# Kernel tuning notes

Hardware: AMD Instinct MI355X
Metric: run time of the kernel (lower is better)

The kernel has to match this reference:

```python
import jax, jax.numpy as jnp
import numpy as np

B, T, I, H, G = 4096, 1024, 1, 16, 48  # G = 3*H gates

def _gru_layer(inp, w_ih, w_hh, b_ih, b_hh):
    # inp: [B, T, Din] -> out: [B, T, H]. PyTorch GRU gate math.
    # Precompute all input-side gate projections once (batched GEMM).
    xg = jnp.einsum('btd,gd->tbg', inp, w_ih) + b_ih  # [T, B, 3H]

    def step(h, xg_t):
        hg = h @ w_hh.T + b_hh                         # [B, 3H]
        xr, xz, xn = jnp.split(xg_t, 3, axis=-1)
        hr, hz, hn = jnp.split(hg, 3, axis=-1)
        r = jax.nn.sigmoid(xr + hr)
        z = jax.nn.sigmoid(xz + hz)
        n = jnp.tanh(xn + r * hn)
        h_new = (1.0 - z) * n + z * h
        return h_new, h_new

    h0 = jnp.zeros((inp.shape[0], H), dtype=inp.dtype)
    _, ys = jax.lax.scan(step, h0, xg)                 # ys: [T, B, H]
    return jnp.transpose(ys, (1, 0, 2))                # [B, T, H]

def setup_inputs() -> dict:
    key = jax.random.key(0)
    ks = jax.random.split(key, 8)
    s = 1.0 / np.sqrt(H)  # PyTorch default uniform(-1/sqrt(H), 1/sqrt(H))
    u = lambda k, shape: jax.random.uniform(k, shape, jnp.float32, -s, s)
    return {
        'x':      jax.random.normal(ks[0], (B, T, I), jnp.float32),
        'w_ih0':  u(ks[1], (G, I)),
        'w_ih12': u(ks[2], (2, G, H)),
        'w_hh':   u(ks[3], (3, G, H)),
        'b_ih':   u(ks[4], (3, G)),
        'b_hh':   u(ks[5], (3, G)),
        'fc_w':   u(ks[6], (5, H)),
        'fc_b':   u(ks[7], (5,)),
    }

def reference(x, w_ih0, w_ih12, w_hh, b_ih, b_hh, fc_w, fc_b):
    # 3-layer GRU (dropout=0.3 between layers is identity in eval mode)
    h = _gru_layer(x, w_ih0,     w_hh[0], b_ih[0], b_hh[0])
    h = _gru_layer(h, w_ih12[0], w_hh[1], b_ih[1], b_hh[1])
    h = _gru_layer(h, w_ih12[1], w_hh[2], b_ih[2], b_hh[2])
    # Linear head on the last timestep
    return h[:, -1, :] @ fc_w.T + fc_b                 # [B, 5]
```

## Files before the change

### kernel.cpp

```cpp
#include <hip/hip_runtime.h>
#include <stdint.h>

#define TSTEPS 1024
#define S 4
#define NK 258
#define L2E 1.4426950408889634f

typedef float v2f __attribute__((ext_vector_type(2)));
typedef float v4f __attribute__((ext_vector_type(4)));

__device__ __forceinline__ float rcpf_(float v) { return __builtin_amdgcn_rcpf(v); }
__device__ __forceinline__ float ex2(float v) { return __builtin_amdgcn_exp2f(v); }
#define PKFMA(a, b, c) __builtin_elementwise_fma((a), (b), (c))

__device__ __forceinline__ v2f ldg2(const float* p) {
    v2f r; uint64_t a = (uint64_t)p;
    asm volatile("global_load_dwordx2 %0, %1, off\n\ts_waitcnt vmcnt(0)"
                 : "=v"(r) : "v"(a));
    return r;
}
__device__ __forceinline__ float ldg1(const float* p) {
    float r; uint64_t a = (uint64_t)p;
    asm volatile("global_load_dword %0, %1, off\n\ts_waitcnt vmcnt(0)"
                 : "=v"(r) : "v"(a));
    return r;
}

#define RDH(dst, p)                                                        \
    do {                                                                   \
        v4f a0 = *(const v4f*)(p);                                         \
        v4f a1 = *(const v4f*)((p) + 4);                                   \
        v4f a2 = *(const v4f*)((p) + 8);                                   \
        v4f a3 = *(const v4f*)((p) + 12);                                  \
        dst[0] = __builtin_shufflevector(a0, a0, 0, 1);                    \
        dst[1] = __builtin_shufflevector(a0, a0, 2, 3);                    \
        dst[2] = __builtin_shufflevector(a1, a1, 0, 1);                    \
        dst[3] = __builtin_shufflevector(a1, a1, 2, 3);                    \
        dst[4] = __builtin_shufflevector(a2, a2, 0, 1);                    \
        dst[5] = __builtin_shufflevector(a2, a2, 2, 3);                    \
        dst[6] = __builtin_shufflevector(a3, a3, 0, 1);                    \
        dst[7] = __builtin_shufflevector(a3, a3, 2, 3);                    \
    } while (0)

#define DOT8(w, h, seed)                                                   \
    ({                                                                     \
        v2f _a = PKFMA(w[0], h[0], (seed));                                \
        _a = PKFMA(w[1], h[1], _a); _a = PKFMA(w[2], h[2], _a);            \
        _a = PKFMA(w[3], h[3], _a); _a = PKFMA(w[4], h[4], _a);            \
        _a = PKFMA(w[5], h[5], _a); _a = PKFMA(w[6], h[6], _a);            \
        _a = PKFMA(w[7], h[7], _a);                                        \
        _a.x + _a.y;                                                       \
    })

__global__ __launch_bounds__(192, 3)
__attribute__((amdgpu_waves_per_eu(3, 3)))
void gru3_po(
    const float* __restrict__ x,
    const float* __restrict__ w_ih0,
    const float* __restrict__ w_ih12,
    const float* __restrict__ w_hh,
    const float* __restrict__ b_ih,
    const float* __restrict__ b_hh,
    const float* __restrict__ fc_w,
    const float* __restrict__ fc_b,
    float* __restrict__ out)
{
    __shared__ float pring[2][2][S][4][48];
    __shared__ float hscr[3][4][16];

    const int tid = threadIdx.x;
    const int role = tid >> 6;
    const int lane = tid & 63;
    const int s = lane >> 4;
    const int u = lane & 15;
    const int seq = blockIdx.x * 4 + s;

    ((float*)hscr)[tid] = 0.f;
    __syncthreads();

    if (role == 0) {
        v2f wr[8], wz[8], wn[8], v1r[8], v1z[8], v1n[8];
#pragma unroll
        for (int m = 0; m < 8; ++m) {
            wr[m] = ldg2(w_hh + (u) * 16 + 2 * m) * -L2E;
            wz[m] = ldg2(w_hh + (16 + u) * 16 + 2 * m) * -L2E;
            wn[m] = ldg2(w_hh + (32 + u) * 16 + 2 * m) * (2.f * L2E);
            v1r[m] = ldg2(w_ih12 + (u) * 16 + 2 * m) * -L2E;
            v1z[m] = ldg2(w_ih12 + (16 + u) * 16 + 2 * m) * -L2E;
            v1n[m] = ldg2(w_ih12 + (32 + u) * 16 + 2 * m) * (2.f * L2E);
        }
        const float wxr = ldg1(w_ih0 + u) * -L2E;
        const float wxz = ldg1(w_ih0 + 16 + u) * -L2E;
        const float wxn = ldg1(w_ih0 + 32 + u) * (2.f * L2E);
        const v2f sbr = {-(ldg1(b_ih + u) + ldg1(b_hh + u)) * L2E, 0.f};
        const v2f sbz = {-(ldg1(b_ih + 16 + u) + ldg1(b_hh + 16 + u)) * L2E, 0.f};
        const v2f sbn = {ldg1(b_hh + 32 + u) * (2.f * L2E), 0.f};
        const float bnx = ldg1(b_ih + 32 + u) * (2.f * L2E);
        const v2f s1r = {-(ldg1(b_ih + 48 + u) + ldg1(b_hh + 48 + u)) * L2E, 0.f};
        const v2f s1z = {-(ldg1(b_ih + 64 + u) + ldg1(b_hh + 64 + u)) * L2E, 0.f};
        const v2f s1x = {ldg1(b_ih + 80 + u) * (2.f * L2E), 0.f};

        const float* xp = x + (size_t)seq * TSTEPS;
        const float* hr = &hscr[0][s][0];
        float* pc = &pring[0][0][0][s][0];
        float* pp = &pring[0][1][0][s][0];
        float hown = 0.f;
        v4f xq = *(const v4f*)xp;
        for (int K = 0; K < NK; ++K) {
            if (K < 256) {
                v4f xqn = *(const v4f*)(xp + 4 * ((K < 255) ? K + 1 : 255));
#pragma unroll
                for (int j = 0; j < S; ++j) {
                    v2f hp[8];
                    RDH(hp, hr);
                    float xt = xq[j];
                    float sr = fmaf(wxr, xt, DOT8(wr, hp, sbr));
                    float sz = fmaf(wxz, xt, DOT8(wz, hp, sbz));
                    float snh = DOT8(wn, hp, sbn);
                    float r = rcpf_(1.f + ex2(sr));
                    float z = rcpf_(1.f + ex2(sz));
                    float ut = fmaf(r, snh, fmaf(wxn, xt, bnx));
                    float n = fmaf(-2.f, rcpf_(ex2(ut) + 1.f), 1.f);
                    hown = fmaf(z, hown - n, n);
                    hscr[0][s][u] = hown;
                    v2f hq[8];
                    RDH(hq, hr);
                    float pr = DOT8(v1r, hq, s1r);
                    float pz = DOT8(v1z, hq, s1z);
                    float px = DOT8(v1n, hq, s1x);
                    float* pb = pc + j * (4 * 48);
                    pb[u] = pr; pb[16 + u] = pz; pb[32 + u] = px;
                }
                xq = xqn;
            }
            __syncthreads();
            float* t_ = pc; pc = pp; pp = t_;
        }
    } else if (role == 1) {
        v2f wr[8], wz[8], wn[8], v2r[8], v2z[8], v2n[8];
#pragma unroll
        for (int m = 0; m < 8; ++m) {
            wr[m] = ldg2(w_hh + (48 + u) * 16 + 2 * m) * -L2E;
            wz[m] = ldg2(w_hh + (48 + 16 + u) * 16 + 2 * m) * -L2E;
            wn[m] = ldg2(w_hh + (48 + 32 + u) * 16 + 2 * m) * (2.f * L2E);
            v2r[m] = ldg2(w_ih12 + (48 + u) * 16 + 2 * m) * -L2E;
            v2z[m] = ldg2(w_ih12 + (48 + 16 + u) * 16 + 2 * m) * -L2E;
            v2n[m] = ldg2(w_ih12 + (48 + 32 + u) * 16 + 2 * m) * (2.f * L2E);
        }
        const v2f sbn = {ldg1(b_hh + 80 + u) * (2.f * L2E), 0.f};
        const v2f s2r = {-(ldg1(b_ih + 96 + u) + ldg1(b_hh + 96 + u)) * L2E, 0.f};
        const v2f s2z = {-(ldg1(b_ih + 112 + u) + ldg1(b_hh + 112 + u)) * L2E, 0.f};
        const v2f s2x = {ldg1(b_ih + 128 + u) * (2.f * L2E), 0.f};

        const float* hr = &hscr[1][s][0];
        const float* in0 = &pring[0][0][0][s][0];
        const float* in1 = &pring[0][1][0][s][0];
        float* my0 = &pring[1][0][0][s][0];
        float* my1 = &pring[1][1][0][s][0];
        const float* inp = in1;
        float* mycur = my0; float* myprv = my1;
        float hown = 0.f;
        for (int K = 0; K < NK; ++K) {
            if (K >= 1 && K < 257) {
#pragma unroll
                for (int j = 0; j < S; ++j) {
                    const float* qb = inp + j * (4 * 48);
                    float pr = qb[u], pz = qb[16 + u], px = qb[32 + u];
                    v2f hp[8];
                    RDH(hp, hr);
                    float sr = DOT8(wr, hp, ((v2f){pr, 0.f}));
                    float sz = DOT8(wz, hp, ((v2f){pz, 0.f}));
                    float snh = DOT8(wn, hp, sbn);
                    float r = rcpf_(1.f + ex2(sr));
                    float z = rcpf_(1.f + ex2(sz));
                    float ut = fmaf(r, snh, px);
                    float n = fmaf(-2.f, rcpf_(ex2(ut) + 1.f), 1.f);
                    hown = fmaf(z, hown - n, n);
                    hscr[1][s][u] = hown;
                    v2f hq[8];
                    RDH(hq, hr);
                    float qr = DOT8(v2r, hq, s2r);
                    float qz = DOT8(v2z, hq, s2z);
                    float qx = DOT8(v2n, hq, s2x);
                    float* pb = mycur + j * (4 * 48);
                    pb[u] = qr; pb[16 + u] = qz; pb[32 + u] = qx;
                }
            }
            __syncthreads();
            const float* t0 = (inp == in0) ? in1 : in0; inp = t0;
            float* t1 = mycur; mycur = myprv; myprv = t1;
        }
    } else {
        v2f wr[8], wz[8], wn[8];
#pragma unroll
        for (int m = 0; m < 8; ++m) {
            wr[m] = ldg2(w_hh + (96 + u) * 16 + 2 * m) * -L2E;
            wz[m] = ldg2(w_hh + (96 + 16 + u) * 16 + 2 * m) * -L2E;
            wn[m] = ldg2(w_hh + (96 + 32 + u) * 16 + 2 * m) * (2.f * L2E);
        }
        const v2f sbn = {ldg1(b_hh + 128 + u) * (2.f * L2E), 0.f};

        const float* hr = &hscr[2][s][0];
        const float* in0 = &pring[1][0][0][s][0];
        const float* in1 = &pring[1][1][0][s][0];
        const float* inp = in1;
        float hown = 0.f;
        for (int K = 0; K < NK; ++K) {
            if (K >= 2) {
#pragma unroll
                for (int j = 0; j < S; ++j) {
                    const float* qb = inp + j * (4 * 48);
                    float pr = qb[u], pz = qb[16 + u], px = qb[32 + u];
                    v2f hp[8];
                    RDH(hp, hr);
                    float sr = DOT8(wr, hp, ((v2f){pr, 0.f}));
                    float sz = DOT8(wz, hp, ((v2f){pz, 0.f}));
                    float snh = DOT8(wn, hp, sbn);
                    float r = rcpf_(1.f + ex2(sr));
                    float z = rcpf_(1.f + ex2(sz));
                    float ut = fmaf(r, snh, px);
                    float n = fmaf(-2.f, rcpf_(ex2(ut) + 1.f), 1.f);
                    hown = fmaf(z, hown - n, n);
                    hscr[2][s][u] = hown;
                }
            }
            __syncthreads();
            const float* t0 = (inp == in0) ? in1 : in0; inp = t0;
        }
        v2f hf[8];
        RDH(hf, hr);
        const int ur = (u < 5) ? u : 0;
        v2f fw[8];
#pragma unroll
        for (int m = 0; m < 8; ++m) fw[m] = ldg2(fc_w + ur * 16 + 2 * m);
        float acc = ldg1(fc_b + ur) + DOT8(fw, hf, ((v2f){0.f, 0.f}));
        if (u < 5) out[seq * 5 + u] = acc;
    }
}

extern "C" void kernel_launch(void* const* d_in, const int* in_sizes, int n_in,
                              void* d_out, int out_size, void* d_ws, size_t ws_size,
                              hipStream_t stream) {
    const float* x      = (const float*)d_in[0];
    const float* w_ih0  = (const float*)d_in[1];
    const float* w_ih12 = (const float*)d_in[2];
    const float* w_hh   = (const float*)d_in[3];
    const float* b_ih   = (const float*)d_in[4];
    const float* b_hh   = (const float*)d_in[5];
    const float* fc_w   = (const float*)d_in[6];
    const float* fc_b   = (const float*)d_in[7];
    float* out = (float*)d_out;

    gru3_po<<<1024, 192, 0, stream>>>(
        x, w_ih0, w_ih12, w_hh, b_ih, b_hh, fc_w, fc_b, out);
}
```

Baseline: 511.8 us.

## Replace block barriers with LDS flag handshakes and a 4-deep ring between layer waves

Each GRU layer runs on its own wavefront. The per-chunk __syncthreads that lock-stepped all three waves is replaced by producer/consumer counters in shared memory, which are spin-polled with s_sleep. The projection ring buffers grow from 2 to 4 slots, so a producer can run up to four chunks ahead of its consumer, which should absorb load imbalance between layers. The cost is polling overhead. Correctness now depends on LDS write visibility through lgkmcnt waits, with no explicit memory fences.

```diff
diff --git a/kernel.cpp b/kernel.cpp
--- a/kernel.cpp
+++ b/kernel.cpp
@@ -3,7 +3,8 @@
 
 #define TSTEPS 1024
 #define S 4
-#define NK 258
+#define NKA 256
+#define RD 4
 #define L2E 1.4426950408889634f
 
 typedef float v2f __attribute__((ext_vector_type(2)));
@@ -12,6 +13,7 @@
 __device__ __forceinline__ float rcpf_(float v) { return __builtin_amdgcn_rcpf(v); }
 __device__ __forceinline__ float ex2(float v) { return __builtin_amdgcn_exp2f(v); }
 #define PKFMA(a, b, c) __builtin_elementwise_fma((a), (b), (c))
+#define LGKM0() asm volatile("s_waitcnt lgkmcnt(0)" ::: "memory")
 
 __device__ __forceinline__ v2f ldg2(const float* p) {
     v2f r; uint64_t a = (uint64_t)p;
@@ -54,7 +56,7 @@
 
 __global__ __launch_bounds__(192, 3)
 __attribute__((amdgpu_waves_per_eu(3, 3)))
-void gru3_po(
+void gru3_async(
     const float* __restrict__ x,
     const float* __restrict__ w_ih0,
     const float* __restrict__ w_ih12,
@@ -65,9 +67,11 @@
     const float* __restrict__ fc_b,
     float* __restrict__ out)
 {
-    __shared__ float pring[2][2][S][4][48];
+    __shared__ float pring[2][RD][S][4][48];
     __shared__ float hscr[3][4][16];
-
+    __shared__ int flg[4];
+
+    volatile int* vf = flg;
     const int tid = threadIdx.x;
     const int role = tid >> 6;
     const int lane = tid & 63;
@@ -76,6 +80,7 @@
     const int seq = blockIdx.x * 4 + s;
 
     ((float*)hscr)[tid] = 0.f;
+    if (tid < 4) flg[tid] = 0;
     __syncthreads();
 
     if (role == 0) {
@@ -102,39 +107,39 @@
 
         const float* xp = x + (size_t)seq * TSTEPS;
         const float* hr = &hscr[0][s][0];
-        float* pc = &pring[0][0][0][s][0];
-        float* pp = &pring[0][1][0][s][0];
+        float* ring0 = &pring[0][0][0][0][0];
         float hown = 0.f;
         v4f xq = *(const v4f*)xp;
-        for (int K = 0; K < NK; ++K) {
-            if (K < 256) {
-                v4f xqn = *(const v4f*)(xp + 4 * ((K < 255) ? K + 1 : 255));
-#pragma unroll
-                for (int j = 0; j < S; ++j) {
-                    v2f hp[8];
-                    RDH(hp, hr);
-                    float xt = xq[j];
-                    float sr = fmaf(wxr, xt, DOT8(wr, hp, sbr));
-                    float sz = fmaf(wxz, xt, DOT8(wz, hp, sbz));
-                    float snh = DOT8(wn, hp, sbn);
-                    float r = rcpf_(1.f + ex2(sr));
-                    float z = rcpf_(1.f + ex2(sz));
-                    float ut = fmaf(r, snh, fmaf(wxn, xt, bnx));
-                    float n = fmaf(-2.f, rcpf_(ex2(ut) + 1.f), 1.f);
-                    hown = fmaf(z, hown - n, n);
-                    hscr[0][s][u] = hown;
-                    v2f hq[8];
-                    RDH(hq, hr);
-                    float pr = DOT8(v1r, hq, s1r);
-                    float pz = DOT8(v1z, hq, s1z);
-                    float px = DOT8(v1n, hq, s1x);
-                    float* pb = pc + j * (4 * 48);
-                    pb[u] = pr; pb[16 + u] = pz; pb[32 + u] = px;
-                }
-                xq = xqn;
+        for (int K = 0; K < NKA; ++K) {
+            while (vf[2] + RD <= K) __builtin_amdgcn_s_sleep(1);
+            v4f xqn = *(const v4f*)(xp + 4 * ((K < 255) ? K + 1 : 255));
+            float* pb = ring0 + (K & (RD - 1)) * 768 + s * 48;
+#pragma unroll
+            for (int j = 0; j < S; ++j) {
+                v2f hp[8];
+                RDH(hp, hr);
+                float xt = xq[j];
+                float sr = fmaf(wxr, xt, DOT8(wr, hp, sbr));
+                float sz = fmaf(wxz, xt, DOT8(wz, hp, sbz));
+                float snh = DOT8(wn, hp, sbn);
+                float r = rcpf_(1.f + ex2(sr));
+                float z = rcpf_(1.f + ex2(sz));
+                float ut = fmaf(r, snh, fmaf(wxn, xt, bnx));
+                float n = fmaf(-2.f, rcpf_(ex2(ut) + 1.f), 1.f);
+                hown = fmaf(z, hown - n, n);
+                hscr[0][s][u] = hown;
+                v2f hq[8];
+                RDH(hq, hr);
+                float pr = DOT8(v1r, hq, s1r);
+                float pz = DOT8(v1z, hq, s1z);
+                float px = DOT8(v1n, hq, s1x);
+                pb[j * 192 + u] = pr;
+                pb[j * 192 + 16 + u] = pz;
+                pb[j * 192 + 32 + u] = px;
             }
-            __syncthreads();
-            float* t_ = pc; pc = pp; pp = t_;
+            xq = xqn;
+            LGKM0();
+            if (tid == 0) vf[0] = K + 1;
         }
     } else if (role == 1) {
         v2f wr[8], wz[8], wn[8], v2r[8], v2z[8], v2n[8];
@@ -153,42 +158,41 @@
         const v2f s2x = {ldg1(b_ih + 128 + u) * (2.f * L2E), 0.f};
 
         const float* hr = &hscr[1][s][0];
-        const float* in0 = &pring[0][0][0][s][0];
-        const float* in1 = &pring[0][1][0][s][0];
-        float* my0 = &pring[1][0][0][s][0];
-        float* my1 = &pring[1][1][0][s][0];
-        const float* inp = in1;
-        float* mycur = my0; float* myprv = my1;
+        const float* ring0 = &pring[0][0][0][0][0];
+        float* ring1 = &pring[1][0][0][0][0];
         float hown = 0.f;
-        for (int K = 0; K < NK; ++K) {
-            if (K >= 1 && K < 257) {
-#pragma unroll
-                for (int j = 0; j < S; ++j) {
-                    const float* qb = inp + j * (4 * 48);
-                    float pr = qb[u], pz = qb[16 + u], px = qb[32 + u];
-                    v2f hp[8];
-                    RDH(hp, hr);
-                    float sr = DOT8(wr, hp, ((v2f){pr, 0.f}));
-                    float sz = DOT8(wz, hp, ((v2f){pz, 0.f}));
-                    float snh = DOT8(wn, hp, sbn);
-                    float r = rcpf_(1.f + ex2(sr));
-                    float z = rcpf_(1.f + ex2(sz));
-                    float ut = fmaf(r, snh, px);
-                    float n = fmaf(-2.f, rcpf_(ex2(ut) + 1.f), 1.f);
-                    hown = fmaf(z, hown - n, n);
-                    hscr[1][s][u] = hown;
-                    v2f hq[8];
-                    RDH(hq, hr);
-                    float qr = DOT8(v2r, hq, s2r);
-                    float qz = DOT8(v2z, hq, s2z);
-                    float qx = DOT8(v2n, hq, s2x);
-                    float* pb = mycur + j * (4 * 48);
-                    pb[u] = qr; pb[16 + u] = qz; pb[32 + u] = qx;
-                }
+        for (int K = 0; K < NKA; ++K) {
+            while (vf[0] < K + 1) __builtin_amdgcn_s_sleep(1);
+            while (vf[3] + RD <= K) __builtin_amdgcn_s_sleep(1);
+            const float* qb = ring0 + (K & (RD - 1)) * 768 + s * 48;
+            float* pb = ring1 + (K & (RD - 1)) * 768 + s * 48;
+#pragma unroll
+            for (int j = 0; j < S; ++j) {
+                float pr = qb[j * 192 + u];
+                float pz = qb[j * 192 + 16 + u];
+                float px = qb[j * 192 + 32 + u];
+                v2f hp[8];
+                RDH(hp, hr);
+                float sr = DOT8(wr, hp, ((v2f){pr, 0.f}));
+                float sz = DOT8(wz, hp, ((v2f){pz, 0.f}));
+                float snh = DOT8(wn, hp, sbn);
+                float r = rcpf_(1.f + ex2(sr));
+                float z = rcpf_(1.f + ex2(sz));
+                float ut = fmaf(r, snh, px);
+                float n = fmaf(-2.f, rcpf_(ex2(ut) + 1.f), 1.f);
+                hown = fmaf(z, hown - n, n);
+                hscr[1][s][u] = hown;
+                v2f hq[8];
+                RDH(hq, hr);
+                float qr = DOT8(v2r, hq, s2r);
+                float qz = DOT8(v2z, hq, s2z);
+                float qx = DOT8(v2n, hq, s2x);
+                pb[j * 192 + u] = qr;
+                pb[j * 192 + 16 + u] = qz;
+                pb[j * 192 + 32 + u] = qx;
             }
-            __syncthreads();
-            const float* t0 = (inp == in0) ? in1 : in0; inp = t0;
-            float* t1 = mycur; mycur = myprv; myprv = t1;
+            LGKM0();
+            if (tid == 64) { vf[2] = K + 1; vf[1] = K + 1; }
         }
     } else {
         v2f wr[8], wz[8], wn[8];
@@ -201,31 +205,30 @@
         const v2f sbn = {ldg1(b_hh + 128 + u) * (2.f * L2E), 0.f};
 
         const float* hr = &hscr[2][s][0];
-        const float* in0 = &pring[1][0][0][s][0];
-        const float* in1 = &pring[1][1][0][s][0];
-        const float* inp = in1;
+        const float* ring1 = &pring[1][0][0][0][0];
         float hown = 0.f;
-        for (int K = 0; K < NK; ++K) {
-            if (K >= 2) {
-#pragma unroll
-                for (int j = 0; j < S; ++j) {
-                    const float* qb = inp + j * (4 * 48);
-                    float pr = qb[u], pz = qb[16 + u], px = qb[32 + u];
-                    v2f hp[8];
-                    RDH(hp, hr);
-                    float sr = DOT8(wr, hp, ((v2f){pr, 0.f}));
-                    float sz = DOT8(wz, hp, ((v2f){pz, 0.f}));
-                    float snh = DOT8(wn, hp, sbn);
-                    float r = rcpf_(1.f + ex2(sr));
-                    float z = rcpf_(1.f + ex2(sz));
-                    float ut = fmaf(r, snh, px);
-                    float n = fmaf(-2.f, rcpf_(ex2(ut) + 1.f), 1.f);
-                    hown = fmaf(z, hown - n, n);
-                    hscr[2][s][u] = hown;
-                }
+        for (int K = 0; K < NKA; ++K) {
+            while (vf[1] < K + 1) __builtin_amdgcn_s_sleep(1);
+            const float* qb = ring1 + (K & (RD - 1)) * 768 + s * 48;
+#pragma unroll
+            for (int j = 0; j < S; ++j) {
+                float pr = qb[j * 192 + u];
+                float pz = qb[j * 192 + 16 + u];
+                float px = qb[j * 192 + 32 + u];
+                v2f hp[8];
+                RDH(hp, hr);
+                float sr = DOT8(wr, hp, ((v2f){pr, 0.f}));
+                float sz = DOT8(wz, hp, ((v2f){pz, 0.f}));
+                float snh = DOT8(wn, hp, sbn);
+                float r = rcpf_(1.f + ex2(sr));
+                float z = rcpf_(1.f + ex2(sz));
+                float ut = fmaf(r, snh, px);
+                float n = fmaf(-2.f, rcpf_(ex2(ut) + 1.f), 1.f);
+                hown = fmaf(z, hown - n, n);
+                hscr[2][s][u] = hown;
             }
-            __syncthreads();
-            const float* t0 = (inp == in0) ? in1 : in0; inp = t0;
+            LGKM0();
+            if (tid == 128) vf[3] = K + 1;
         }
         v2f hf[8];
         RDH(hf, hr);
@@ -251,6 +254,6 @@
     const float* fc_b   = (const float*)d_in[7];
     float* out = (float*)d_out;
 
-    gru3_po<<<1024, 192, 0, stream>>>(
+    gru3_async<<<1024, 192, 0, stream>>>(
         x, w_ih0, w_ih12, w_hh, b_ih, b_hh, fc_w, fc_b, out);
 }
```

Result: slower. 525.6 us (+2.7%).

## Split each hidden unit's dot products across lane pairs with DPP reduction

Applied to the files above, without the earlier changes.

Each hidden unit is now handled by two lanes, each doing half of the 16-wide dot products, with the partial sums combined through a DPP lane swap. The sigmoid work for r and z is split between the pair and exchanged the same way. Each block now covers 2 sequences instead of 4, the grid doubles, and launch bounds allow 6 blocks per SM. The aim is a shorter serial dependency chain per timestep and more waves to hide latency, at the cost of extra DPP and select instructions and the same number of barriers per sequence.

```diff
diff --git a/kernel.cpp b/kernel.cpp
--- a/kernel.cpp
+++ b/kernel.cpp
@@ -12,6 +12,15 @@
 __device__ __forceinline__ float rcpf_(float v) { return __builtin_amdgcn_rcpf(v); }
 __device__ __forceinline__ float ex2(float v) { return __builtin_amdgcn_exp2f(v); }
 #define PKFMA(a, b, c) __builtin_elementwise_fma((a), (b), (c))
+
+__device__ __forceinline__ float dpp_x1(float v) {
+    return __int_as_float(__builtin_amdgcn_update_dpp(
+        0, __float_as_int(v), 0xB1, 0xF, 0xF, true));
+}
+__device__ __forceinline__ float pairsum(v2f a) {
+    float s = a.x + a.y;
+    return s + dpp_x1(s);
+}
 
 __device__ __forceinline__ v2f ldg2(const float* p) {
     v2f r; uint64_t a = (uint64_t)p;
@@ -26,35 +35,20 @@
     return r;
 }
 
-#define RDH(dst, p)                                                        \
+#define CH4(W, H, SEED) \
+    PKFMA(W[3], H[3], PKFMA(W[2], H[2], PKFMA(W[1], H[1], PKFMA(W[0], H[0], (SEED)))))
+
+#define RD2(dst, p)                                                        \
     do {                                                                   \
         v4f a0 = *(const v4f*)(p);                                         \
         v4f a1 = *(const v4f*)((p) + 4);                                   \
-        v4f a2 = *(const v4f*)((p) + 8);                                   \
-        v4f a3 = *(const v4f*)((p) + 12);                                  \
         dst[0] = __builtin_shufflevector(a0, a0, 0, 1);                    \
         dst[1] = __builtin_shufflevector(a0, a0, 2, 3);                    \
         dst[2] = __builtin_shufflevector(a1, a1, 0, 1);                    \
         dst[3] = __builtin_shufflevector(a1, a1, 2, 3);                    \
-        dst[4] = __builtin_shufflevector(a2, a2, 0, 1);                    \
-        dst[5] = __builtin_shufflevector(a2, a2, 2, 3);                    \
-        dst[6] = __builtin_shufflevector(a3, a3, 0, 1);                    \
-        dst[7] = __builtin_shufflevector(a3, a3, 2, 3);                    \
     } while (0)
 
-#define DOT8(w, h, seed)                                                   \
-    ({                                                                     \
-        v2f _a = PKFMA(w[0], h[0], (seed));                                \
-        _a = PKFMA(w[1], h[1], _a); _a = PKFMA(w[2], h[2], _a);            \
-        _a = PKFMA(w[3], h[3], _a); _a = PKFMA(w[4], h[4], _a);            \
-        _a = PKFMA(w[5], h[5], _a); _a = PKFMA(w[6], h[6], _a);            \
-        _a = PKFMA(w[7], h[7], _a);                                        \
-        _a.x + _a.y;                                                       \
-    })
-
-__global__ __launch_bounds__(192, 3)
-__attribute__((amdgpu_waves_per_eu(3, 3)))
-void gru3_po(
+__global__ __launch_bounds__(192, 6) void gru3_rs32(
     const float* __restrict__ x,
     const float* __restrict__ w_ih0,
     const float* __restrict__ w_ih12,
@@ -65,176 +59,203 @@
     const float* __restrict__ fc_b,
     float* __restrict__ out)
 {
-    __shared__ float pring[2][2][S][4][48];
-    __shared__ float hscr[3][4][16];
+    __shared__ float pring[2][2][S][2][48];
+    __shared__ float hrec[3][2][16];
 
     const int tid = threadIdx.x;
     const int role = tid >> 6;
-    const int lane = tid & 63;
-    const int s = lane >> 4;
-    const int u = lane & 15;
-    const int seq = blockIdx.x * 4 + s;
-
-    ((float*)hscr)[tid] = 0.f;
+    const int l63 = tid & 63;
+    const int s = l63 >> 5;
+    const int l31 = l63 & 31;
+    const int u = l31 >> 1;
+    const int c = l31 & 1;
+    const int c8 = c * 8;
+    const int seq = blockIdx.x * 2 + s;
+    const v2f zz = {0.f, 0.f};
+
+    if (tid < 96) ((float*)hrec)[tid] = 0.f;
     __syncthreads();
 
     if (role == 0) {
-        v2f wr[8], wz[8], wn[8], v1r[8], v1z[8], v1n[8];
-#pragma unroll
-        for (int m = 0; m < 8; ++m) {
-            wr[m] = ldg2(w_hh + (u) * 16 + 2 * m) * -L2E;
-            wz[m] = ldg2(w_hh + (16 + u) * 16 + 2 * m) * -L2E;
-            wn[m] = ldg2(w_hh + (32 + u) * 16 + 2 * m) * (2.f * L2E);
-            v1r[m] = ldg2(w_ih12 + (u) * 16 + 2 * m) * -L2E;
-            v1z[m] = ldg2(w_ih12 + (16 + u) * 16 + 2 * m) * -L2E;
-            v1n[m] = ldg2(w_ih12 + (32 + u) * 16 + 2 * m) * (2.f * L2E);
+        v2f wr[4], wz[4], wn[4], vr[4], vz[4], vn[4];
+#pragma unroll
+        for (int m = 0; m < 4; ++m) {
+            wr[m] = ldg2(w_hh + (u) * 16 + c8 + 2 * m) * -L2E;
+            wz[m] = ldg2(w_hh + (16 + u) * 16 + c8 + 2 * m) * -L2E;
+            wn[m] = ldg2(w_hh + (32 + u) * 16 + c8 + 2 * m) * (2.f * L2E);
+            vr[m] = ldg2(w_ih12 + (u) * 16 + c8 + 2 * m) * -L2E;
+            vz[m] = ldg2(w_ih12 + (16 + u) * 16 + c8 + 2 * m) * -L2E;
+            vn[m] = ldg2(w_ih12 + (32 + u) * 16 + c8 + 2 * m) * (2.f * L2E);
         }
         const float wxr = ldg1(w_ih0 + u) * -L2E;
         const float wxz = ldg1(w_ih0 + 16 + u) * -L2E;
         const float wxn = ldg1(w_ih0 + 32 + u) * (2.f * L2E);
-        const v2f sbr = {-(ldg1(b_ih + u) + ldg1(b_hh + u)) * L2E, 0.f};
-        const v2f sbz = {-(ldg1(b_ih + 16 + u) + ldg1(b_hh + 16 + u)) * L2E, 0.f};
-        const v2f sbn = {ldg1(b_hh + 32 + u) * (2.f * L2E), 0.f};
+        const v2f sbr = {c ? 0.f : -(ldg1(b_ih + u) + ldg1(b_hh + u)) * L2E, 0.f};
+        const v2f sbz = {c ? 0.f : -(ldg1(b_ih + 16 + u) + ldg1(b_hh + 16 + u)) * L2E, 0.f};
+        const v2f sbn = {c ? 0.f : ldg1(b_hh + 32 + u) * (2.f * L2E), 0.f};
         const float bnx = ldg1(b_ih + 32 + u) * (2.f * L2E);
-        const v2f s1r = {-(ldg1(b_ih + 48 + u) + ldg1(b_hh + 48 + u)) * L2E, 0.f};
-        const v2f s1z = {-(ldg1(b_ih + 64 + u) + ldg1(b_hh + 64 + u)) * L2E, 0.f};
-        const v2f s1x = {ldg1(b_ih + 80 + u) * (2.f * L2E), 0.f};
+        const v2f s1r = {c ? 0.f : -(ldg1(b_ih + 48 + u) + ldg1(b_hh + 48 + u)) * L2E, 0.f};
+        const v2f s1z = {c ? 0.f : -(ldg1(b_ih + 64 + u) + ldg1(b_hh + 64 + u)) * L2E, 0.f};
+        const v2f s1x = {c ? 0.f : ldg1(b_ih + 80 + u) * (2.f * L2E), 0.f};
 
         const float* xp = x + (size_t)seq * TSTEPS;
-        const float* hr = &hscr[0][s][0];
-        float* pc = &pring[0][0][0][s][0];
-        float* pp = &pring[0][1][0][s][0];
+        float* hw = &hrec[0][s][u];
+        const float* hr = &hrec[0][s][c8];
+        float* rw0 = &pring[0][0][0][s][0];
+        float* rw1 = &pring[0][1][0][s][0];
+        v2f hrep[4] = {zz, zz, zz, zz};
         float hown = 0.f;
-        v4f xq = *(const v4f*)xp;
         for (int K = 0; K < NK; ++K) {
             if (K < 256) {
-                v4f xqn = *(const v4f*)(xp + 4 * ((K < 255) ? K + 1 : 255));
+                v4f xq = *(const v4f*)(xp + 4 * K);
+                float* pb = rw0;
 #pragma unroll
                 for (int j = 0; j < S; ++j) {
-                    v2f hp[8];
-                    RDH(hp, hr);
                     float xt = xq[j];
-                    float sr = fmaf(wxr, xt, DOT8(wr, hp, sbr));
-                    float sz = fmaf(wxz, xt, DOT8(wz, hp, sbz));
-                    float snh = DOT8(wn, hp, sbn);
-                    float r = rcpf_(1.f + ex2(sr));
-                    float z = rcpf_(1.f + ex2(sz));
+                    v2f a;
+                    a = CH4(wr, hrep, sbr);
+                    float sr = fmaf(wxr, xt, pairsum(a));
+                    a = CH4(wz, hrep, sbz);
+                    float sz = fmaf(wxz, xt, pairsum(a));
+                    a = CH4(wn, hrep, sbn);
+                    float snh = pairsum(a);
+                    float p = c ? sz : sr;
+                    float sg = rcpf_(1.f + ex2(p));
+                    float og = dpp_x1(sg);
+                    float r = c ? og : sg, z = c ? sg : og;
                     float ut = fmaf(r, snh, fmaf(wxn, xt, bnx));
                     float n = fmaf(-2.f, rcpf_(ex2(ut) + 1.f), 1.f);
                     hown = fmaf(z, hown - n, n);
-                    hscr[0][s][u] = hown;
-                    v2f hq[8];
-                    RDH(hq, hr);
-                    float pr = DOT8(v1r, hq, s1r);
-                    float pz = DOT8(v1z, hq, s1z);
-                    float px = DOT8(v1n, hq, s1x);
-                    float* pb = pc + j * (4 * 48);
+                    *hw = hown;
+                    RD2(hrep, hr);
+                    a = CH4(vr, hrep, s1r);
+                    float pr = pairsum(a);
+                    a = CH4(vz, hrep, s1z);
+                    float pz = pairsum(a);
+                    a = CH4(vn, hrep, s1x);
+                    float px = pairsum(a);
                     pb[u] = pr; pb[16 + u] = pz; pb[32 + u] = px;
+                    pb += 96;
                 }
-                xq = xqn;
             }
             __syncthreads();
-            float* t_ = pc; pc = pp; pp = t_;
+            float* t_ = rw0; rw0 = rw1; rw1 = t_;
         }
     } else if (role == 1) {
-        v2f wr[8], wz[8], wn[8], v2r[8], v2z[8], v2n[8];
-#pragma unroll
-        for (int m = 0; m < 8; ++m) {
-            wr[m] = ldg2(w_hh + (48 + u) * 16 + 2 * m) * -L2E;
-            wz[m] = ldg2(w_hh + (48 + 16 + u) * 16 + 2 * m) * -L2E;
-            wn[m] = ldg2(w_hh + (48 + 32 + u) * 16 + 2 * m) * (2.f * L2E);
-            v2r[m] = ldg2(w_ih12 + (48 + u) * 16 + 2 * m) * -L2E;
-            v2z[m] = ldg2(w_ih12 + (48 + 16 + u) * 16 + 2 * m) * -L2E;
-            v2n[m] = ldg2(w_ih12 + (48 + 32 + u) * 16 + 2 * m) * (2.f * L2E);
-        }
-        const v2f sbn = {ldg1(b_hh + 80 + u) * (2.f * L2E), 0.f};
-        const v2f s2r = {-(ldg1(b_ih + 96 + u) + ldg1(b_hh + 96 + u)) * L2E, 0.f};
-        const v2f s2z = {-(ldg1(b_ih + 112 + u) + ldg1(b_hh + 112 + u)) * L2E, 0.f};
-        const v2f s2x = {ldg1(b_ih + 128 + u) * (2.f * L2E), 0.f};
-
-        const float* hr = &hscr[1][s][0];
-        const float* in0 = &pring[0][0][0][s][0];
-        const float* in1 = &pring[0][1][0][s][0];
-        float* my0 = &pring[1][0][0][s][0];
-        float* my1 = &pring[1][1][0][s][0];
-        const float* inp = in1;
-        float* mycur = my0; float* myprv = my1;
+        v2f wr[4], wz[4], wn[4], vr[4], vz[4], vn[4];
+#pragma unroll
+        for (int m = 0; m < 4; ++m) {
+            wr[m] = ldg2(w_hh + (48 + u) * 16 + c8 + 2 * m) * -L2E;
+            wz[m] = ldg2(w_hh + (48 + 16 + u) * 16 + c8 + 2 * m) * -L2E;
+            wn[m] = ldg2(w_hh + (48 + 32 + u) * 16 + c8 + 2 * m) * (2.f * L2E);
+            vr[m] = ldg2(w_ih12 + (48 + u) * 16 + c8 + 2 * m) * -L2E;
+            vz[m] = ldg2(w_ih12 + (48 + 16 + u) * 16 + c8 + 2 * m) * -L2E;
+            vn[m] = ldg2(w_ih12 + (48 + 32 + u) * 16 + c8 + 2 * m) * (2.f * L2E);
+        }
+        const v2f sbn = {c ? 0.f : ldg1(b_hh + 80 + u) * (2.f * L2E), 0.f};
+        const v2f s2r = {c ? 0.f : -(ldg1(b_ih + 96 + u) + ldg1(b_hh + 96 + u)) * L2E, 0.f};
+        const v2f s2z = {c ? 0.f : -(ldg1(b_ih + 112 + u) + ldg1(b_hh + 112 + u)) * L2E, 0.f};
+        const v2f s2x = {c ? 0.f : ldg1(b_ih + 128 + u) * (2.f * L2E), 0.f};
+
+        float* hw = &hrec[1][s][u];
+        const float* hr = &hrec[1][s][c8];
+        const float* ri0 = &pring[0][0][0][s][0];
+        const float* ri1 = &pring[0][1][0][s][0];
+        float* ro0 = &pring[1][0][0][s][0];
+        float* ro1 = &pring[1][1][0][s][0];
+        const float* rin = ri1;
+        v2f hrep[4] = {zz, zz, zz, zz};
         float hown = 0.f;
         for (int K = 0; K < NK; ++K) {
             if (K >= 1 && K < 257) {
+                const float* qb = rin;
+                float* pb = ro0;
 #pragma unroll
                 for (int j = 0; j < S; ++j) {
-                    const float* qb = inp + j * (4 * 48);
                     float pr = qb[u], pz = qb[16 + u], px = qb[32 + u];
-                    v2f hp[8];
-                    RDH(hp, hr);
-                    float sr = DOT8(wr, hp, ((v2f){pr, 0.f}));
-                    float sz = DOT8(wz, hp, ((v2f){pz, 0.f}));
-                    float snh = DOT8(wn, hp, sbn);
-                    float r = rcpf_(1.f + ex2(sr));
-                    float z = rcpf_(1.f + ex2(sz));
+                    v2f a;
+                    a = CH4(wr, hrep, zz);
+                    float sr = pr + pairsum(a);
+                    a = CH4(wz, hrep, zz);
+                    float sz = pz + pairsum(a);
+                    a = CH4(wn, hrep, sbn);
+                    float snh = pairsum(a);
+                    float p = c ? sz : sr;
+                    float sg = rcpf_(1.f + ex2(p));
+                    float og = dpp_x1(sg);
+                    float r = c ? og : sg, z = c ? sg : og;
                     float ut = fmaf(r, snh, px);
                     float n = fmaf(-2.f, rcpf_(ex2(ut) + 1.f), 1.f);
                     hown = fmaf(z, hown - n, n);
-                    hscr[1][s][u] = hown;
-                    v2f hq[8];
-                    RDH(hq, hr);
-                    float qr = DOT8(v2r, hq, s2r);
-                    float qz = DOT8(v2z, hq, s2z);
-                    float qx = DOT8(v2n, hq, s2x);
-                    float* pb = mycur + j * (4 * 48);
+                    *hw = hown;
+                    RD2(hrep, hr);
+                    a = CH4(vr, hrep, s2r);
+                    float qr = pairsum(a);
+                    a = CH4(vz, hrep, s2z);
+                    float qz = pairsum(a);
+                    a = CH4(vn, hrep, s2x);
+                    float qx = pairsum(a);
                     pb[u] = qr; pb[16 + u] = qz; pb[32 + u] = qx;
+                    pb += 96; qb += 96;
                 }
             }
             __syncthreads();
-            const float* t0 = (inp == in0) ? in1 : in0; inp = t0;
-            float* t1 = mycur; mycur = myprv; myprv = t1;
+            const float* t0 = (rin == ri0) ? ri1 : ri0; rin = t0;
+            float* t1 = ro0; ro0 = ro1; ro1 = t1;
         }
     } else {
-        v2f wr[8], wz[8], wn[8];
-#pragma unroll
-        for (int m = 0; m < 8; ++m) {
-            wr[m] = ldg2(w_hh + (96 + u) * 16 + 2 * m) * -L2E;
-            wz[m] = ldg2(w_hh + (96 + 16 + u) * 16 + 2 * m) * -L2E;
-            wn[m] = ldg2(w_hh + (96 + 32 + u) * 16 + 2 * m) * (2.f * L2E);
-        }
-        const v2f sbn = {ldg1(b_hh + 128 + u) * (2.f * L2E), 0.f};
-
-        const float* hr = &hscr[2][s][0];
-        const float* in0 = &pring[1][0][0][s][0];
-        const float* in1 = &pring[1][1][0][s][0];
-        const float* inp = in1;
+        v2f wr[4], wz[4], wn[4];
+#pragma unroll
+        for (int m = 0; m < 4; ++m) {
+            wr[m] = ldg2(w_hh + (96 + u) * 16 + c8 + 2 * m) * -L2E;
+            wz[m] = ldg2(w_hh + (96 + 16 + u) * 16 + c8 + 2 * m) * -L2E;
+            wn[m] = ldg2(w_hh + (96 + 32 + u) * 16 + c8 + 2 * m) * (2.f * L2E);
+        }
+        const v2f sbn = {c ? 0.f : ldg1(b_hh + 128 + u) * (2.f * L2E), 0.f};
+
+        float* hw = &hrec[2][s][u];
+        const float* hr = &hrec[2][s][c8];
+        const float* ri0 = &pring[1][0][0][s][0];
+        const float* ri1 = &pring[1][1][0][s][0];
+        const float* rin = ri1;
+        v2f hrep[4] = {zz, zz, zz, zz};
         float hown = 0.f;
         for (int K = 0; K < NK; ++K) {
             if (K >= 2) {
+                const float* qb = rin;
 #pragma unroll
                 for (int j = 0; j < S; ++j) {
-                    const float* qb = inp + j * (4 * 48);
                     float pr = qb[u], pz = qb[16 + u], px = qb[32 + u];
-                    v2f hp[8];
-                    RDH(hp, hr);
-                    float sr = DOT8(wr, hp, ((v2f){pr, 0.f}));
-                    float sz = DOT8(wz, hp, ((v2f){pz, 0.f}));
-                    float snh = DOT8(wn, hp, sbn);
-                    float r = rcpf_(1.f + ex2(sr));
-                    float z = rcpf_(1.f + ex2(sz));
+                    v2f a;
+                    a = CH4(wr, hrep, zz);
+                    float sr = pr + pairsum(a);
+                    a = CH4(wz, hrep, zz);
+                    float sz = pz + pairsum(a);
+                    a = CH4(wn, hrep, sbn);
+                    float snh = pairsum(a);
+                    float p = c ? sz : sr;
+                    float sg = rcpf_(1.f + ex2(p));
+                    float og = dpp_x1(sg);
+                    float r = c ? og : sg, z = c ? sg : og;
                     float ut = fmaf(r, snh, px);
                     float n = fmaf(-2.f, rcpf_(ex2(ut) + 1.f), 1.f);
                     hown = fmaf(z, hown - n, n);
-                    hscr[2][s][u] = hown;
+                    *hw = hown;
+                    RD2(hrep, hr);
+                    qb += 96;
                 }
             }
             __syncthreads();
-            const float* t0 = (inp == in0) ? in1 : in0; inp = t0;
-        }
-        v2f hf[8];
-        RDH(hf, hr);
+            const float* t0 = (rin == ri0) ? ri1 : ri0; rin = t0;
+        }
         const int ur = (u < 5) ? u : 0;
-        v2f fw[8];
-#pragma unroll
-        for (int m = 0; m < 8; ++m) fw[m] = ldg2(fc_w + ur * 16 + 2 * m);
-        float acc = ldg1(fc_b + ur) + DOT8(fw, hf, ((v2f){0.f, 0.f}));
-        if (u < 5) out[seq * 5 + u] = acc;
+        v2f fw[4];
+#pragma unroll
+        for (int m = 0; m < 4; ++m) fw[m] = ldg2(fc_w + ur * 16 + c8 + 2 * m);
+        const v2f fb = {c ? 0.f : ldg1(fc_b + ur), 0.f};
+        v2f a = CH4(fw, hrep, fb);
+        float acc = pairsum(a);
+        if (u < 5 && c == 0) out[seq * 5 + u] = acc;
     }
 }
 
@@ -251,6 +272,6 @@
     const float* fc_b   = (const float*)d_in[7];
     float* out = (float*)d_out;
 
-    gru3_po<<<1024, 192, 0, stream>>>(
+    gru3_rs32<<<2048, 192, 0, stream>>>(
         x, w_ih0, w_ih12, w_hh, b_ih, b_hh, fc_w, fc_b, out);
 }
```

Result: slower. 1.715 ms (+235.2%).
